# Kernel tuning notes

Hardware: AMD Instinct MI355X
Metric: run time of the kernel (lower is better)

## Reference

```python
import jax, jax.numpy as jnp
import numpy as np

EPS = 1e-6

def _l2norm(t):
    # F.normalize over channel axis (axis=1) of (B, dk, L)
    n = jnp.sqrt(jnp.sum(t * t, axis=1, keepdims=True))
    return t / jnp.maximum(n, EPS)

def setup_inputs() -> dict:
    key = jax.random.key(0)
    ks = jax.random.split(key, 8)
    B, Cin, Cenc, dk, dv, H, W = 2, 64, 96, 64, 64, 96, 96
    return {
        "x": jax.random.normal(ks[0], (B, Cin, H, W), dtype=jnp.float32),
        "x_enc": jax.random.normal(ks[1], (B, Cenc, H, W), dtype=jnp.float32),
        "Wq": jax.random.normal(ks[2], (dk, Cenc), dtype=jnp.float32) * 0.05,
        "bq": jax.random.normal(ks[3], (dk,), dtype=jnp.float32) * 0.05,
        "Wk": jax.random.normal(ks[4], (dk, Cenc), dtype=jnp.float32) * 0.05,
        "bk": jax.random.normal(ks[5], (dk,), dtype=jnp.float32) * 0.05,
        "Wv": jax.random.normal(ks[6], (dv, Cin), dtype=jnp.float32) * 0.05,
        "bv": jax.random.normal(ks[7], (dv,), dtype=jnp.float32) * 0.05,
    }

def reference(x, x_enc, Wq, bq, Wk, bk, Wv, bv):
    B, _, H, W = x.shape
    L = H * W
    # 1x1 conv projections == channel matmuls, then flatten spatial dims
    Q = (jnp.einsum('bchw,kc->bkhw', x_enc, Wq) + bq[None, :, None, None]).reshape(B, -1, L)
    K = (jnp.einsum('bchw,kc->bkhw', x_enc, Wk) + bk[None, :, None, None]).reshape(B, -1, L)
    V = (jnp.einsum('bchw,kc->bkhw', x, Wv) + bv[None, :, None, None]).reshape(B, -1, L)
    # per-position L2 normalization over the dk channel axis ('l2' mode)
    Q = _l2norm(Q)
    K = _l2norm(K)
    # A[b,i,j] = sum_q Q[b,q,i] * K[b,q,j], softmax over j
    A = jax.nn.softmax(jnp.einsum('bqi,bqj->bij', Q, K), axis=-1)  # (B, L, L)
    R = jnp.einsum('bij,bvj->bvi', A, V)  # (B, dv, L)
    return R.reshape(B, -1, H, W)
```

## Files before the change

### kernel.cpp

```cpp
#include <hip/hip_runtime.h>
#include <hip/hip_bf16.h>
#include <math.h>

#define NB   2
#define CIN  64
#define CENC 96
#define DK   64
#define DV   64
#define LL   9216
#define QBLK 256
#define KVBLK 64
#define NQT  (LL/QBLK)
#define LOG2E 1.44269504088896340736f

typedef __attribute__((ext_vector_type(8)))  short short8;
typedef __attribute__((ext_vector_type(16))) float f32x16;
typedef __attribute__((ext_vector_type(2)))  unsigned int uint2v;
typedef unsigned int uint;

__device__ inline void gload16(const void* g, void* l) {
    __builtin_amdgcn_global_load_lds(
        (const __attribute__((address_space(1))) unsigned int*)g,
        (__attribute__((address_space(3))) unsigned int*)l, 16, 0, 0);
}

__device__ inline unsigned short f2bf(float f) {
    union { float f; uint u; } v; v.f = f;
    uint r = (v.u + 0x7FFFu + ((v.u >> 16) & 1u)) >> 16;
    return (unsigned short)r;
}

__device__ inline uint pack_bf16x2(float lo, float hi) {
    __hip_bfloat162 h = __float22bfloat162_rn(float2{lo, hi});
    union { __hip_bfloat162 h; uint u; } cvt; cvt.h = h;
    return cvt.u;
}

__device__ inline void plswap(uint& a, uint& b) {
#if __has_builtin(__builtin_amdgcn_permlane32_swap)
    uint2v r = __builtin_amdgcn_permlane32_swap(a, b, false, false);
    a = r.x; b = r.y;
#else
    const int lane = threadIdx.x & 63;
    uint t = (lane < 32) ? b : a;
    t = __shfl_xor(t, 32, 64);
    uint an = (lane < 32) ? a : t;
    uint bn = (lane < 32) ? t : b;
    a = an; b = bn;
#endif
}

__global__ __launch_bounds__(256) void proj_kernel(
    const float* __restrict__ x, const float* __restrict__ x_enc,
    const float* __restrict__ Wq, const float* __restrict__ bq,
    const float* __restrict__ Wk, const float* __restrict__ bk,
    const float* __restrict__ Wv, const float* __restrict__ bv,
    unsigned short* __restrict__ Qb, unsigned short* __restrict__ Kb,
    unsigned short* __restrict__ Vt, int nqk)
{
    __shared__ float sh[2 * CENC * 64];
    const int tid = threadIdx.x;

    if ((int)blockIdx.x < nqk) {
        float* Wt0 = sh;
        float* Wt1 = sh + CENC * 64;
        for (int idx = tid; idx < DK * CENC; idx += 256) {
            int k = idx / CENC, c = idx - k * CENC;
            Wt0[c * 64 + (k ^ (c & 31))] = Wq[idx];
            Wt1[c * 64 + (k ^ (c & 31))] = Wk[idx];
        }
        __syncthreads();

        const int w    = __builtin_amdgcn_readfirstlane(tid >> 6);
        const int lane = tid & 63;
        const int gw   = blockIdx.x * 4 + w;
        const int p0g  = gw * 16;
        const int b    = p0g / LL;
        const int p0   = p0g - b * LL;

        float qa[16], ka[16];
        const float bqv = bq[lane], bkv = bk[lane];
#pragma unroll
        for (int p = 0; p < 16; ++p) { qa[p] = bqv; ka[p] = bkv; }

        const float* xp = x_enc + (size_t)b * CENC * LL + p0;
#pragma unroll 4
        for (int c = 0; c < CENC; ++c) {
            const float wq = Wt0[c * 64 + (lane ^ (c & 31))];
            const float wk = Wt1[c * 64 + (lane ^ (c & 31))];
            const float* xc = xp + (size_t)c * LL;
#pragma unroll
            for (int p = 0; p < 16; ++p) {
                const float xv = xc[p];
                qa[p] = fmaf(wq, xv, qa[p]);
                ka[p] = fmaf(wk, xv, ka[p]);
            }
        }

        unsigned short* qrow = Qb + (size_t)(b * LL + p0) * 64 + lane;
        unsigned short* krow = Kb + (size_t)(b * LL + p0) * 64 + lane;
#pragma unroll
        for (int p = 0; p < 16; ++p) {
            float sq = qa[p] * qa[p];
            float sk = ka[p] * ka[p];
#pragma unroll
            for (int m = 1; m < 64; m <<= 1) {
                sq += __shfl_xor(sq, m, 64);
                sk += __shfl_xor(sk, m, 64);
            }
            qrow[(size_t)p * 64] = f2bf(qa[p] * (LOG2E / fmaxf(sqrtf(sq), 1e-6f)));
            krow[(size_t)p * 64] = f2bf(ka[p] * (1.f / fmaxf(sqrtf(sk), 1e-6f)));
        }
    } else {
        float* Wt = sh;
        unsigned short* Vsh = (unsigned short*)(sh + CIN * 64);
        for (int idx = tid; idx < DV * CIN; idx += 256) {
            int v = idx / CIN, c = idx - v * CIN;
            Wt[c * 64 + (v ^ (c & 31))] = Wv[idx];
        }
        __syncthreads();

        const int w    = __builtin_amdgcn_readfirstlane(tid >> 6);
        const int lane = tid & 63;
        const int l0g  = ((int)blockIdx.x - nqk) * 64;
        const int b    = l0g / LL;
        const int l0   = l0g - b * LL;
        const int p0   = w * 16;

        float va[16];
        const float bvv = bv[lane];
#pragma unroll
        for (int p = 0; p < 16; ++p) va[p] = bvv;

        const float* xp = x + (size_t)b * CIN * LL + l0 + p0;
#pragma unroll 4
        for (int c = 0; c < CIN; ++c) {
            const float wv = Wt[c * 64 + (lane ^ (c & 31))];
            const float* xc = xp + (size_t)c * LL;
#pragma unroll
            for (int p = 0; p < 16; ++p) va[p] = fmaf(wv, xc[p], va[p]);
        }
#pragma unroll
        for (int p = 0; p < 16; ++p) Vsh[(p0 + p) * 64 + lane] = f2bf(va[p]);
        __syncthreads();

        const int v = tid & 63, w2 = tid >> 6;
        uint pk[8];
#pragma unroll
        for (int j = 0; j < 8; ++j)
            pk[j] = (uint)Vsh[(w2 * 16 + 2 * j) * 64 + v] |
                    ((uint)Vsh[(w2 * 16 + 2 * j + 1) * 64 + v] << 16);
        uint4* dst = (uint4*)(Vt + (size_t)b * 64 * LL + (size_t)v * LL + l0 + w2 * 16);
        dst[0] = make_uint4(pk[0], pk[1], pk[2], pk[3]);
        dst[1] = make_uint4(pk[4], pk[5], pk[6], pk[7]);
    }
}

__global__ __launch_bounds__(256, 2) void flash_kernel(
    const unsigned short* __restrict__ Qb,
    const unsigned short* __restrict__ Kb,
    const unsigned short* __restrict__ Vt,
    float* __restrict__ Sp, float* __restrict__ Rp,
    int JS, int nt)
{
    __shared__ unsigned short Kl[2][KVBLK * 64];
    __shared__ unsigned short Vl[2][64 * KVBLK];

    const int bid0  = blockIdx.x;
    const int chunk = gridDim.x >> 3;
    const int bid   = (bid0 & 7) * chunk + (bid0 >> 3);

    const int qt  = bid % NQT;
    const int js  = (bid / NQT) % JS;
    const int b   = bid / (NQT * JS);
    const int tid = threadIdx.x;
    const int w = tid >> 6, lane = tid & 63;
    const int ln = lane & 31, h = lane >> 5;
    const int i0w = qt * QBLK + w * 64;

    short8 qf[2][4];
#pragma unroll
    for (int ig = 0; ig < 2; ++ig)
#pragma unroll
        for (int kc = 0; kc < 4; ++kc)
            qf[ig][kc] = *(const short8*)(Qb + ((size_t)(b * LL + i0w + ig * 32 + ln)) * 64 + kc * 16 + h * 8);

    const int o0 = w * 1024 + lane * 16;
    const int o1 = o0 + 4096;
    const int r0 = o0 >> 7, r1 = o1 >> 7;
    const int c0 = ((o0 >> 4) & 7) ^ (r0 & 7);
    const int c1 = ((o1 >> 4) & 7) ^ (r1 & 7);

    const unsigned short* KbB = Kb + (size_t)b * LL * 64;
    const unsigned short* VtB = Vt + (size_t)b * 64 * LL;

    f32x16 racc[2][2];
#pragma unroll
    for (int ig = 0; ig < 2; ++ig)
#pragma unroll
        for (int vg = 0; vg < 2; ++vg)
#pragma unroll
            for (int r = 0; r < 16; ++r) racc[ig][vg][r] = 0.f;
    float ssum[2] = {0.f, 0.f};

    int j0 = js * nt * KVBLK;
    gload16(KbB + (size_t)(j0 + r0) * 64 + c0 * 8, (char*)Kl[0] + w * 1024);
    gload16(KbB + (size_t)(j0 + r1) * 64 + c1 * 8, (char*)Kl[0] + w * 1024 + 4096);
    gload16(VtB + (size_t)r0 * LL + j0 + c0 * 8, (char*)Vl[0] + w * 1024);
    gload16(VtB + (size_t)r1 * LL + j0 + c1 * 8, (char*)Vl[0] + w * 1024 + 4096);

    for (int t = 0; t < nt; ++t, j0 += KVBLK) {
        __syncthreads();
        const int bb = t & 1;
        if (t + 1 < nt) {
            const int j1 = j0 + KVBLK;
            gload16(KbB + (size_t)(j1 + r0) * 64 + c0 * 8, (char*)Kl[bb ^ 1] + w * 1024);
            gload16(KbB + (size_t)(j1 + r1) * 64 + c1 * 8, (char*)Kl[bb ^ 1] + w * 1024 + 4096);
            gload16(VtB + (size_t)r0 * LL + j1 + c0 * 8, (char*)Vl[bb ^ 1] + w * 1024);
            gload16(VtB + (size_t)r1 * LL + j1 + c1 * 8, (char*)Vl[bb ^ 1] + w * 1024 + 4096);
        }
        const char* Klb = (const char*)Kl[bb];
        const char* Vlb = (const char*)Vl[bb];

#pragma unroll
        for (int jt = 0; jt < 2; ++jt) {
            f32x16 sacc[2];
#pragma unroll
            for (int ig = 0; ig < 2; ++ig)
#pragma unroll
                for (int r = 0; r < 16; ++r) sacc[ig][r] = 0.f;

            __builtin_amdgcn_s_setprio(1);
#pragma unroll
            for (int kc = 0; kc < 4; ++kc) {
                const int rowK = jt * 32 + ln;
                const short8 kf = *(const short8*)(Klb + rowK * 128 + (((kc << 1) + h) ^ (rowK & 7)) * 16);
                sacc[0] = __builtin_amdgcn_mfma_f32_32x32x16_bf16(kf, qf[0][kc], sacc[0], 0, 0, 0);
                sacc[1] = __builtin_amdgcn_mfma_f32_32x32x16_bf16(kf, qf[1][kc], sacc[1], 0, 0, 0);
            }
            __builtin_amdgcn_s_setprio(0);

            short8 pf[2][2];
#pragma unroll
            for (int ig = 0; ig < 2; ++ig) {
                float p[16];
#pragma unroll
                for (int r = 0; r < 16; ++r) p[r] = __builtin_amdgcn_exp2f(sacc[ig][r]);
                float s0 = 0.f;
#pragma unroll
                for (int r = 0; r < 16; r += 4) s0 += (p[r] + p[r + 1]) + (p[r + 2] + p[r + 3]);
                ssum[ig] += s0;
                uint u0[4], u1[4];
#pragma unroll
                for (int g = 0; g < 4; ++g) {
                    u0[g] = pack_bf16x2(p[4 * g], p[4 * g + 1]);
                    u1[g] = pack_bf16x2(p[4 * g + 2], p[4 * g + 3]);
                }
#pragma unroll
                for (int c = 0; c < 2; ++c) {
                    uint a0 = u0[2 * c], b0 = u0[2 * c + 1];
                    uint a1 = u1[2 * c], b1 = u1[2 * c + 1];
                    plswap(a0, b0);
                    plswap(a1, b1);
                    union { uint u[4]; short8 s; } P;
                    P.u[0] = a0; P.u[1] = a1; P.u[2] = b0; P.u[3] = b1;
                    pf[ig][c] = P.s;
                }
            }

            __builtin_amdgcn_s_setprio(1);
#pragma unroll
            for (int c = 0; c < 2; ++c) {
                const int kcv = 2 * jt + c;
#pragma unroll
                for (int vg = 0; vg < 2; ++vg) {
                    const int rowV = vg * 32 + ln;
                    const short8 vf = *(const short8*)(Vlb + rowV * 128 + (((kcv << 1) + h) ^ (rowV & 7)) * 16);
                    racc[0][vg] = __builtin_amdgcn_mfma_f32_32x32x16_bf16(pf[0][c], vf, racc[0][vg], 0, 0, 0);
                    racc[1][vg] = __builtin_amdgcn_mfma_f32_32x32x16_bf16(pf[1][c], vf, racc[1][vg], 0, 0, 0);
                }
            }
            __builtin_amdgcn_s_setprio(0);
        }
    }

#pragma unroll
    for (int ig = 0; ig < 2; ++ig) {
        float s = ssum[ig] + __shfl_xor(ssum[ig], 32, 64);
        if (h == 0) Sp[(size_t)(b * JS + js) * LL + i0w + ig * 32 + ln] = s;
    }
    const size_t rBase = (size_t)(b * JS + js) * 64;
#pragma unroll
    for (int ig = 0; ig < 2; ++ig)
#pragma unroll
        for (int vg = 0; vg < 2; ++vg) {
            float* dst = Rp + (rBase + vg * 32 + ln) * (size_t)LL + i0w + ig * 32 + 4 * h;
#pragma unroll
            for (int rr = 0; rr < 4; ++rr) {
                float4 val = make_float4(racc[ig][vg][4 * rr + 0], racc[ig][vg][4 * rr + 1],
                                         racc[ig][vg][4 * rr + 2], racc[ig][vg][4 * rr + 3]);
                *(float4*)&dst[8 * rr] = val;
            }
        }
}

__global__ __launch_bounds__(256) void combine_kernel(
    const float* __restrict__ Sp, const float* __restrict__ Rp,
    float* __restrict__ out, int JS)
{
    size_t g4 = ((size_t)blockIdx.x * 256 + threadIdx.x) * 4;
    int l = (int)(g4 % LL);
    int v = (int)((g4 / LL) % 64);
    int b = (int)(g4 / ((size_t)64 * LL));
    float4 s = make_float4(0.f, 0.f, 0.f, 0.f);
    float4 r = make_float4(0.f, 0.f, 0.f, 0.f);
    for (int js = 0; js < JS; ++js) {
        const float4 sv = *(const float4*)&Sp[(size_t)(b * JS + js) * LL + l];
        const float4 rv = *(const float4*)&Rp[((size_t)(b * JS + js) * 64 + v) * LL + l];
        s.x += sv.x; s.y += sv.y; s.z += sv.z; s.w += sv.w;
        r.x += rv.x; r.y += rv.y; r.z += rv.z; r.w += rv.w;
    }
    *(float4*)&out[g4] = make_float4(r.x / s.x, r.y / s.y, r.z / s.z, r.w / s.w);
}

extern "C" void kernel_launch(void* const* d_in, const int* in_sizes, int n_in,
                              void* d_out, int out_size, void* d_ws, size_t ws_size,
                              hipStream_t stream) {
    (void)in_sizes; (void)n_in; (void)out_size;
    const float* x     = (const float*)d_in[0];
    const float* x_enc = (const float*)d_in[1];
    const float* Wq    = (const float*)d_in[2];
    const float* bq    = (const float*)d_in[3];
    const float* Wk    = (const float*)d_in[4];
    const float* bk    = (const float*)d_in[5];
    const float* Wv    = (const float*)d_in[6];
    const float* bv    = (const float*)d_in[7];
    float* out = (float*)d_out;
    char* ws = (char*)d_ws;

    const size_t nBF = (size_t)NB * LL * 64 * 2;
    unsigned short* Qb = (unsigned short*)ws;
    unsigned short* Kb = (unsigned short*)(ws + nBF);
    unsigned short* Vt = (unsigned short*)(ws + 2 * nBF);

    int JS = 12;
    {
        const int cand[3] = {12, 8, 4};
        for (int ci = 0; ci < 3; ++ci) {
            JS = cand[ci];
            size_t need = 3 * nBF + (size_t)NB * JS * LL * 4 + (size_t)NB * JS * 64 * LL * 4;
            if (need <= ws_size) break;
        }
    }
    float* Sp = (float*)(ws + 3 * nBF);
    float* Rp = Sp + (size_t)NB * JS * LL;
    int nt = (LL / JS) / KVBLK;

    const int nqk = NB * LL / 64;
    proj_kernel  <<<2 * nqk, 256, 0, stream>>>(x, x_enc, Wq, bq, Wk, bk, Wv, bv, Qb, Kb, Vt, nqk);
    flash_kernel <<<NB * JS * NQT, 256, 0, stream>>>(Qb, Kb, Vt, Sp, Rp, JS, nt);
    combine_kernel<<<(NB * 64 * LL) / 1024, 256, 0, stream>>>(Sp, Rp, out, JS);
}
```

Measured before the change: 109.0 us.

## Load K/V directly from global, store bf16 partials, raise occupancy and split

Removes the LDS double-buffered staging of K and V tiles and has each wave read its MFMA fragments straight from global memory. The goal is to eliminate block barriers and LDS usage so three blocks fit per CU. Partial R outputs are stored as bf16 to halve write and combine-read traffic, and the KV split count candidates are raised. Risks include exposed global load latency with no prefetch, redundant loads across waves, and reduced precision in the partial sums.

```diff
diff --git a/kernel.cpp b/kernel.cpp
--- a/kernel.cpp
+++ b/kernel.cpp
@@ -18,16 +18,14 @@
 typedef __attribute__((ext_vector_type(2)))  unsigned int uint2v;
 typedef unsigned int uint;
 
-__device__ inline void gload16(const void* g, void* l) {
-    __builtin_amdgcn_global_load_lds(
-        (const __attribute__((address_space(1))) unsigned int*)g,
-        (__attribute__((address_space(3))) unsigned int*)l, 16, 0, 0);
-}
-
 __device__ inline unsigned short f2bf(float f) {
     union { float f; uint u; } v; v.f = f;
     uint r = (v.u + 0x7FFFu + ((v.u >> 16) & 1u)) >> 16;
     return (unsigned short)r;
+}
+
+__device__ inline float bf2f(uint u) {
+    union { uint u; float f; } c; c.u = u << 16; return c.f;
 }
 
 __device__ inline uint pack_bf16x2(float lo, float hi) {
@@ -156,16 +154,13 @@
     }
 }
 
-__global__ __launch_bounds__(256, 2) void flash_kernel(
+__global__ __launch_bounds__(256, 3) void flash_kernel(
     const unsigned short* __restrict__ Qb,
     const unsigned short* __restrict__ Kb,
     const unsigned short* __restrict__ Vt,
-    float* __restrict__ Sp, float* __restrict__ Rp,
+    float* __restrict__ Sp, unsigned short* __restrict__ Rp,
     int JS, int nt)
 {
-    __shared__ unsigned short Kl[2][KVBLK * 64];
-    __shared__ unsigned short Vl[2][64 * KVBLK];
-
     const int bid0  = blockIdx.x;
     const int chunk = gridDim.x >> 3;
     const int bid   = (bid0 & 7) * chunk + (bid0 >> 3);
@@ -185,15 +180,6 @@
         for (int kc = 0; kc < 4; ++kc)
             qf[ig][kc] = *(const short8*)(Qb + ((size_t)(b * LL + i0w + ig * 32 + ln)) * 64 + kc * 16 + h * 8);
 
-    const int o0 = w * 1024 + lane * 16;
-    const int o1 = o0 + 4096;
-    const int r0 = o0 >> 7, r1 = o1 >> 7;
-    const int c0 = ((o0 >> 4) & 7) ^ (r0 & 7);
-    const int c1 = ((o1 >> 4) & 7) ^ (r1 & 7);
-
-    const unsigned short* KbB = Kb + (size_t)b * LL * 64;
-    const unsigned short* VtB = Vt + (size_t)b * 64 * LL;
-
     f32x16 racc[2][2];
 #pragma unroll
     for (int ig = 0; ig < 2; ++ig)
@@ -203,25 +189,12 @@
             for (int r = 0; r < 16; ++r) racc[ig][vg][r] = 0.f;
     float ssum[2] = {0.f, 0.f};
 
-    int j0 = js * nt * KVBLK;
-    gload16(KbB + (size_t)(j0 + r0) * 64 + c0 * 8, (char*)Kl[0] + w * 1024);
-    gload16(KbB + (size_t)(j0 + r1) * 64 + c1 * 8, (char*)Kl[0] + w * 1024 + 4096);
-    gload16(VtB + (size_t)r0 * LL + j0 + c0 * 8, (char*)Vl[0] + w * 1024);
-    gload16(VtB + (size_t)r1 * LL + j0 + c1 * 8, (char*)Vl[0] + w * 1024 + 4096);
-
-    for (int t = 0; t < nt; ++t, j0 += KVBLK) {
-        __syncthreads();
-        const int bb = t & 1;
-        if (t + 1 < nt) {
-            const int j1 = j0 + KVBLK;
-            gload16(KbB + (size_t)(j1 + r0) * 64 + c0 * 8, (char*)Kl[bb ^ 1] + w * 1024);
-            gload16(KbB + (size_t)(j1 + r1) * 64 + c1 * 8, (char*)Kl[bb ^ 1] + w * 1024 + 4096);
-            gload16(VtB + (size_t)r0 * LL + j1 + c0 * 8, (char*)Vl[bb ^ 1] + w * 1024);
-            gload16(VtB + (size_t)r1 * LL + j1 + c1 * 8, (char*)Vl[bb ^ 1] + w * 1024 + 4096);
-        }
-        const char* Klb = (const char*)Kl[bb];
-        const char* Vlb = (const char*)Vl[bb];
-
+    const int j0 = js * nt * KVBLK;
+    const unsigned short* Kp = Kb + ((size_t)b * LL + j0 + ln) * 64 + h * 8;
+    const unsigned short* Vp0 = Vt + ((size_t)b * 64 + ln) * LL + j0 + h * 8;
+    const unsigned short* Vp1 = Vp0 + (size_t)32 * LL;
+
+    for (int t = 0; t < nt; ++t, Kp += KVBLK * 64, Vp0 += KVBLK, Vp1 += KVBLK) {
 #pragma unroll
         for (int jt = 0; jt < 2; ++jt) {
             f32x16 sacc[2];
@@ -233,8 +206,7 @@
             __builtin_amdgcn_s_setprio(1);
 #pragma unroll
             for (int kc = 0; kc < 4; ++kc) {
-                const int rowK = jt * 32 + ln;
-                const short8 kf = *(const short8*)(Klb + rowK * 128 + (((kc << 1) + h) ^ (rowK & 7)) * 16);
+                const short8 kf = *(const short8*)(Kp + jt * 32 * 64 + kc * 16);
                 sacc[0] = __builtin_amdgcn_mfma_f32_32x32x16_bf16(kf, qf[0][kc], sacc[0], 0, 0, 0);
                 sacc[1] = __builtin_amdgcn_mfma_f32_32x32x16_bf16(kf, qf[1][kc], sacc[1], 0, 0, 0);
             }
@@ -271,11 +243,10 @@
             __builtin_amdgcn_s_setprio(1);
 #pragma unroll
             for (int c = 0; c < 2; ++c) {
-                const int kcv = 2 * jt + c;
+                const int joff = (2 * jt + c) * 16;
 #pragma unroll
                 for (int vg = 0; vg < 2; ++vg) {
-                    const int rowV = vg * 32 + ln;
-                    const short8 vf = *(const short8*)(Vlb + rowV * 128 + (((kcv << 1) + h) ^ (rowV & 7)) * 16);
+                    const short8 vf = *(const short8*)((vg ? Vp1 : Vp0) + joff);
                     racc[0][vg] = __builtin_amdgcn_mfma_f32_32x32x16_bf16(pf[0][c], vf, racc[0][vg], 0, 0, 0);
                     racc[1][vg] = __builtin_amdgcn_mfma_f32_32x32x16_bf16(pf[1][c], vf, racc[1][vg], 0, 0, 0);
                 }
@@ -294,18 +265,19 @@
     for (int ig = 0; ig < 2; ++ig)
 #pragma unroll
         for (int vg = 0; vg < 2; ++vg) {
-            float* dst = Rp + (rBase + vg * 32 + ln) * (size_t)LL + i0w + ig * 32 + 4 * h;
+            unsigned short* dst = Rp + (rBase + vg * 32 + ln) * (size_t)LL + i0w + ig * 32 + 4 * h;
 #pragma unroll
             for (int rr = 0; rr < 4; ++rr) {
-                float4 val = make_float4(racc[ig][vg][4 * rr + 0], racc[ig][vg][4 * rr + 1],
-                                         racc[ig][vg][4 * rr + 2], racc[ig][vg][4 * rr + 3]);
-                *(float4*)&dst[8 * rr] = val;
+                uint2v val;
+                val.x = pack_bf16x2(racc[ig][vg][4 * rr + 0], racc[ig][vg][4 * rr + 1]);
+                val.y = pack_bf16x2(racc[ig][vg][4 * rr + 2], racc[ig][vg][4 * rr + 3]);
+                *(uint2v*)&dst[8 * rr] = val;
             }
         }
 }
 
 __global__ __launch_bounds__(256) void combine_kernel(
-    const float* __restrict__ Sp, const float* __restrict__ Rp,
+    const float* __restrict__ Sp, const unsigned short* __restrict__ Rp,
     float* __restrict__ out, int JS)
 {
     size_t g4 = ((size_t)blockIdx.x * 256 + threadIdx.x) * 4;
@@ -316,9 +288,10 @@
     float4 r = make_float4(0.f, 0.f, 0.f, 0.f);
     for (int js = 0; js < JS; ++js) {
         const float4 sv = *(const float4*)&Sp[(size_t)(b * JS + js) * LL + l];
-        const float4 rv = *(const float4*)&Rp[((size_t)(b * JS + js) * 64 + v) * LL + l];
+        const uint2v rv = *(const uint2v*)&Rp[((size_t)(b * JS + js) * 64 + v) * LL + l];
         s.x += sv.x; s.y += sv.y; s.z += sv.z; s.w += sv.w;
-        r.x += rv.x; r.y += rv.y; r.z += rv.z; r.w += rv.w;
+        r.x += bf2f(rv.x & 0xffffu); r.y += bf2f(rv.x >> 16);
+        r.z += bf2f(rv.y & 0xffffu); r.w += bf2f(rv.y >> 16);
     }
     *(float4*)&out[g4] = make_float4(r.x / s.x, r.y / s.y, r.z / s.z, r.w / s.w);
 }
@@ -343,21 +316,21 @@
     unsigned short* Kb = (unsigned short*)(ws + nBF);
     unsigned short* Vt = (unsigned short*)(ws + 2 * nBF);
 
-    int JS = 12;
+    int JS = 8;
     {
-        const int cand[3] = {12, 8, 4};
+        const int cand[3] = {16, 12, 8};
         for (int ci = 0; ci < 3; ++ci) {
             JS = cand[ci];
-            size_t need = 3 * nBF + (size_t)NB * JS * LL * 4 + (size_t)NB * JS * 64 * LL * 4;
+            size_t need = 3 * nBF + (size_t)NB * JS * LL * 4 + (size_t)NB * JS * 64 * LL * 2;
             if (need <= ws_size) break;
         }
     }
     float* Sp = (float*)(ws + 3 * nBF);
-    float* Rp = Sp + (size_t)NB * JS * LL;
+    unsigned short* Rp = (unsigned short*)(ws + 3 * nBF + (size_t)NB * JS * LL * 4);
     int nt = (LL / JS) / KVBLK;
 
     const int nqk = NB * LL / 64;
-    proj_kernel  <<<2 * nqk, 256, 0, stream>>>(x, x_enc, Wq, bq, Wk, bk, Wv, bv, Qb, Kb, Vt, nqk);
-    flash_kernel <<<NB * JS * NQT, 256, 0, stream>>>(Qb, Kb, Vt, Sp, Rp, JS, nt);
+    proj_kernel   <<<2 * nqk, 256, 0, stream>>>(x, x_enc, Wq, bq, Wk, bk, Wv, bv, Qb, Kb, Vt, nqk);
+    flash_kernel  <<<NB * JS * NQT, 256, 0, stream>>>(Qb, Kb, Vt, Sp, Rp, JS, nt);
     combine_kernel<<<(NB * 64 * LL) / 1024, 256, 0, stream>>>(Sp, Rp, out, JS);
 }
```

Measured after the change: 254.0 us. 2.33x slower.
